# Performance work log

Measured on AMD Instinct MI355X. Metric: run time of the kernel, lower is better.

Reference implementation:

```python
import jax, jax.numpy as jnp
import numpy as np

IN_CH = 128
QK_CH = IN_CH // 8  # 16


def setup_inputs() -> dict:
    key = jax.random.key(0)
    ks = jax.random.split(key, 8)
    B, C, W, H = 8, IN_CH, 64, 64
    x = jax.random.normal(ks[0], (B, C, W, H), dtype=jnp.float32)
    s = 1.0 / np.sqrt(C)
    Wq = jax.random.normal(ks[1], (QK_CH, C), dtype=jnp.float32) * s
    bq = jnp.zeros((QK_CH,), dtype=jnp.float32)
    Wk = jax.random.normal(ks[2], (QK_CH, C), dtype=jnp.float32) * s
    bk = jnp.zeros((QK_CH,), dtype=jnp.float32)
    Wv = jax.random.normal(ks[3], (C, C), dtype=jnp.float32) * s
    bv = jnp.zeros((C,), dtype=jnp.float32)
    gamma = jnp.zeros((1,), dtype=jnp.float32)
    return {"x": x, "Wq": Wq, "bq": bq, "Wk": Wk, "bk": bk, "Wv": Wv, "bv": bv, "gamma": gamma}


def reference(x, Wq, bq, Wk, bk, Wv, bv, gamma):
    B, C, W, H = x.shape
    N = W * H
    xf = x.reshape(B, C, N)  # [B,C,N] tokens along spatial dims
    # 1x1 convs == per-pixel linear projections
    q = jnp.einsum('oc,bcn->bno', Wq, xf) + bq          # [B,N,Cq]
    k = jnp.einsum('oc,bcn->bon', Wk, xf) + bk[:, None]  # [B,Cq,N]
    v = jnp.einsum('oc,bcn->bon', Wv, xf) + bv[:, None]  # [B,C,N]
    scale = jnp.sqrt(jnp.asarray(Wq.shape[0], dtype=x.dtype))
    attn = jax.nn.softmax(jnp.einsum('bno,bom->bnm', q, k) / scale, axis=-1)  # [B,N,N]
    # out[b,c,i] = sum_j v[b,c,j] * attn[b,i,j]  (torch: bmm(value, attention^T))
    out = jnp.einsum('bcj,bij->bci', v, attn).reshape(B, C, W, H)
    return gamma[0] * out + x
```

## Files before the change

kernel.cpp:

```cpp
#include <hip/hip_runtime.h>
#include <cstddef>
#include <cstdint>

#define NTOK 4096
#define NB_  8

typedef float f32x4  __attribute__((ext_vector_type(4)));
typedef float f32x16 __attribute__((ext_vector_type(16)));
typedef short s16x8  __attribute__((ext_vector_type(8)));

static __device__ __forceinline__ unsigned short f2bf(float f) {
    unsigned u = __float_as_uint(f);
    unsigned r = (u + 0x7FFFu + ((u >> 16) & 1u)) >> 16;
    return (unsigned short)r;
}
static __device__ __forceinline__ unsigned packbf2(float a, float b) {
    const unsigned ua = __float_as_uint(a) + 0x8000u;
    const unsigned ub = __float_as_uint(b) + 0x8000u;
    return __builtin_amdgcn_perm(ub, ua, 0x07060302u);
}

__global__ __launch_bounds__(256) void wcvt_kernel(
    const float* __restrict__ Wq, const float* __restrict__ Wk, const float* __restrict__ Wv,
    unsigned short* __restrict__ wvb, unsigned short* __restrict__ wqb,
    unsigned short* __restrict__ wkb)
{
    int i = blockIdx.x * 256 + threadIdx.x;
    if (i < 16384)      wvb[i]         = f2bf(Wv[i]);
    else if (i < 18432) wqb[i - 16384] = f2bf(Wq[i - 16384]);
    else                wkb[i - 18432] = f2bf(Wk[i - 18432]);
}

__global__ __launch_bounds__(256) void proj_kernel(
    const float* __restrict__ x,
    const unsigned short* __restrict__ wvb, const unsigned short* __restrict__ wqb,
    const unsigned short* __restrict__ wkb,
    const float* __restrict__ bq, const float* __restrict__ bk, const float* __restrict__ bv,
    unsigned short* __restrict__ qb, unsigned short* __restrict__ kb,
    unsigned short* __restrict__ vt)
{
    __shared__ float lt[128][68];
    const int t = threadIdx.x;
    const int w = t >> 6, lane = t & 63;
    const int c16 = lane & 15, g16 = lane >> 4;
    const int b  = blockIdx.x & 7;
    const int n0 = (blockIdx.x >> 3) * 64;

    {
        const int n4 = t & 15;
#pragma unroll
        for (int pass = 0; pass < 8; ++pass) {
            const int c = (t >> 4) + 16 * pass;
            const float4 val = ((const float4*)(x + ((size_t)b * 128 + c) * NTOK + n0))[n4];
            *(float4*)&lt[c][n4 * 4] = val;
        }
    }
    __syncthreads();

    const int nl = 16 * w + c16;
    s16x8 xf[4];
#pragma unroll
    for (int kc = 0; kc < 4; ++kc) {
        unsigned rr[8];
#pragma unroll
        for (int i = 0; i < 8; ++i) {
            const unsigned u = __float_as_uint(lt[32 * kc + 8 * g16 + i][nl]);
            rr[i] = u + 0x7FFFu + ((u >> 16) & 1u);
        }
        union { s16x8 v; unsigned u[4]; } cvt;
#pragma unroll
        for (int d = 0; d < 4; ++d)
            cvt.u[d] = __builtin_amdgcn_perm(rr[2 * d + 1], rr[2 * d], 0x07060302u);
        xf[kc] = cvt.v;
    }

    unsigned short* vwp = vt + (size_t)b * (NTOK * 128) +
                          (size_t)(((n0 >> 6) * 8) + 2 * w + (c16 >> 3)) * 1024 + (c16 & 7);
#pragma unroll
    for (int mt = 0; mt < 8; ++mt) {
        f32x4 acc = {0.f, 0.f, 0.f, 0.f};
#pragma unroll
        for (int kc = 0; kc < 4; ++kc) {
            const s16x8 wf = *(const s16x8*)(wvb + (size_t)(16 * mt + c16) * 128 + 32 * kc + 8 * g16);
            acc = __builtin_amdgcn_mfma_f32_16x16x32_bf16(wf, xf[kc], acc, 0, 0, 0);
        }
        const float4 bvv = *(const float4*)(bv + 16 * mt + 4 * g16);
#pragma unroll
        for (int r = 0; r < 4; ++r) {
            const int c = 16 * mt + 4 * g16 + r;
            vwp[c * 8] = f2bf(acc[r] + ((const float*)&bvv)[r]);
        }
    }
    f32x4 aq = {0.f, 0.f, 0.f, 0.f}, ak = {0.f, 0.f, 0.f, 0.f};
#pragma unroll
    for (int kc = 0; kc < 4; ++kc) {
        const s16x8 wqf = *(const s16x8*)(wqb + (size_t)c16 * 128 + 32 * kc + 8 * g16);
        const s16x8 wkf = *(const s16x8*)(wkb + (size_t)c16 * 128 + 32 * kc + 8 * g16);
        aq = __builtin_amdgcn_mfma_f32_16x16x32_bf16(xf[kc], wqf, aq, 0, 0, 0);
        ak = __builtin_amdgcn_mfma_f32_16x16x32_bf16(xf[kc], wkf, ak, 0, 0, 0);
    }
    const float bqv = bq[c16], bkv = bk[c16];
#pragma unroll
    for (int r = 0; r < 4; ++r) {
        const int n = n0 + 16 * w + 4 * g16 + r;
        qb[((size_t)b * NTOK + n) * 16 + c16] = f2bf(0.25f * (aq[r] + bqv));
        kb[((size_t)b * NTOK + n) * 16 + c16] = f2bf(ak[r] + bkv);
    }
}

__global__ __launch_bounds__(256, 2) void flash_kernel(
    const unsigned short* __restrict__ qb, const unsigned short* __restrict__ kb,
    const unsigned short* __restrict__ vt, const float* __restrict__ x,
    const float* __restrict__ gamma, float* __restrict__ out)
{
    __shared__ float smem[4256];

    const int t = threadIdx.x;
    const int w = t >> 6, lane = t & 63;
    const int m31 = lane & 31, h = lane >> 5;
    const int b  = blockIdx.x & 7;
    const int m0 = (blockIdx.x >> 3) * 32;

    const unsigned short* kbb = kb + ((size_t)b * NTOK + w * 1024) * 16;
    const unsigned short* vtb = vt + (size_t)b * (NTOK * 128) + (size_t)w * 16 * 8192 +
                                h * 1024 + m31 * 8;

    const s16x8 qf = *(const s16x8*)(qb + ((size_t)b * NTOK + m0 + m31) * 16 + 8 * h);

    f32x16 O[4];
#pragma unroll
    for (int ct = 0; ct < 4; ++ct)
#pragma unroll
        for (int r = 0; r < 16; ++r) O[ct][r] = 0.f;
    float l_acc = 0.f;

    s16x8 kf0 = *(const s16x8*)(kbb + (size_t)m31 * 16 + 8 * h);
    s16x8 kf1 = *(const s16x8*)(kbb + (size_t)(32 + m31) * 16 + 8 * h);

    const int xaddr = (lane ^ 32) << 2;

    for (int jt = 0; jt < 16; ++jt) {
        const int j0 = jt * 64;

        s16x8 vf[4][4];
#pragma unroll
        for (int s = 0; s < 4; ++s)
#pragma unroll
            for (int ct = 0; ct < 4; ++ct)
                vf[ct][s] = *(const s16x8*)(vtb + jt * 8192 + s * 2048 + ct * 256);

        f32x16 sd[2];
#pragma unroll
        for (int r = 0; r < 16; ++r) { sd[0][r] = 0.f; sd[1][r] = 0.f; }
        sd[0] = __builtin_amdgcn_mfma_f32_32x32x16_bf16(kf0, qf, sd[0], 0, 0, 0);
        sd[1] = __builtin_amdgcn_mfma_f32_32x32x16_bf16(kf1, qf, sd[1], 0, 0, 0);

        if (jt < 15) {
            kf0 = *(const s16x8*)(kbb + (size_t)(j0 + 64 + m31) * 16 + 8 * h);
            kf1 = *(const s16x8*)(kbb + (size_t)(j0 + 96 + m31) * 16 + 8 * h);
        }

#pragma unroll
        for (int t2 = 0; t2 < 2; ++t2)
#pragma unroll
            for (int r = 0; r < 16; ++r) {
                const float e = __expf(sd[t2][r]);
                sd[t2][r] = e;
                l_acc += e;
            }

        uint2 pk[2][4];
#pragma unroll
        for (int t2 = 0; t2 < 2; ++t2)
#pragma unroll
            for (int q = 0; q < 4; ++q) {
                pk[t2][q].x = packbf2(sd[t2][4 * q + 0], sd[t2][4 * q + 1]);
                pk[t2][q].y = packbf2(sd[t2][4 * q + 2], sd[t2][4 * q + 3]);
            }

        uint2 ex[2][2];
#pragma unroll
        for (int t2 = 0; t2 < 2; ++t2)
#pragma unroll
            for (int s1 = 0; s1 < 2; ++s1) {
                const uint2 snd = h ? pk[t2][2 * s1] : pk[t2][2 * s1 + 1];
                ex[t2][s1].x = (unsigned)__builtin_amdgcn_ds_bpermute(xaddr, (int)snd.x);
                ex[t2][s1].y = (unsigned)__builtin_amdgcn_ds_bpermute(xaddr, (int)snd.y);
            }

        s16x8 pf[4];
#pragma unroll
        for (int s = 0; s < 4; ++s) {
            const int t2 = s >> 1, s1 = s & 1;
            const uint2 lo = h ? ex[t2][s1] : pk[t2][2 * s1];
            const uint2 hi = h ? pk[t2][2 * s1 + 1] : ex[t2][s1];
            union { s16x8 v; unsigned u[4]; } asm_;
            asm_.u[0] = lo.x; asm_.u[1] = lo.y; asm_.u[2] = hi.x; asm_.u[3] = hi.y;
            pf[s] = asm_.v;
        }

#pragma unroll
        for (int s = 0; s < 4; ++s)
#pragma unroll
            for (int ct = 0; ct < 4; ++ct)
                O[ct] = __builtin_amdgcn_mfma_f32_32x32x16_bf16(vf[ct][s], pf[s], O[ct], 0, 0, 0);
    }

    l_acc += __shfl_xor(l_acc, 32);

    float* ob = smem;
    float* lb = smem + 4224;
#pragma unroll 1
    for (int src = 1; src < 4; ++src) {
        __syncthreads();
        if (w == src) {
#pragma unroll
            for (int ct = 0; ct < 4; ++ct)
#pragma unroll
                for (int r = 0; r < 16; ++r) {
                    const int c = 32 * ct + (r & 3) + 8 * (r >> 2) + 4 * h;
                    ob[c * 33 + m31] = O[ct][r];
                }
            if (lane < 32) lb[lane] = l_acc;
        }
        __syncthreads();
        if (w == 0) {
#pragma unroll
            for (int ct = 0; ct < 4; ++ct)
#pragma unroll
                for (int r = 0; r < 16; ++r) {
                    const int c = 32 * ct + (r & 3) + 8 * (r >> 2) + 4 * h;
                    O[ct][r] += ob[c * 33 + m31];
                }
            l_acc += lb[m31];
        }
    }

    if (w == 0) {
        const float linv = 1.f / l_acc;
        const float g = gamma[0];
#pragma unroll
        for (int ct = 0; ct < 4; ++ct)
#pragma unroll
            for (int r = 0; r < 16; ++r) {
                const int c = 32 * ct + (r & 3) + 8 * (r >> 2) + 4 * h;
                const size_t idx = ((size_t)b * 128 + c) * NTOK + m0 + m31;
                out[idx] = fmaf(g, O[ct][r] * linv, x[idx]);
            }
    }
}

extern "C" void kernel_launch(void* const* d_in, const int* in_sizes, int n_in,
                              void* d_out, int out_size, void* d_ws, size_t ws_size,
                              hipStream_t stream)
{
    const float* x     = (const float*)d_in[0];
    const float* Wq    = (const float*)d_in[1];
    const float* bq    = (const float*)d_in[2];
    const float* Wk    = (const float*)d_in[3];
    const float* bk    = (const float*)d_in[4];
    const float* Wv    = (const float*)d_in[5];
    const float* bv    = (const float*)d_in[6];
    const float* gamma = (const float*)d_in[7];
    float* out = (float*)d_out;

    unsigned short* qb  = (unsigned short*)d_ws;
    unsigned short* kb  = qb  + (size_t)NB_ * NTOK * 16;
    unsigned short* vt  = kb  + (size_t)NB_ * NTOK * 16;
    unsigned short* wvb = vt  + (size_t)NB_ * 128 * NTOK;
    unsigned short* wqb = wvb + 16384;
    unsigned short* wkb = wqb + 2048;

    wcvt_kernel<<<80, 256, 0, stream>>>(Wq, Wk, Wv, wvb, wqb, wkb);
    proj_kernel<<<512, 256, 0, stream>>>(x, wvb, wqb, wkb, bq, bk, bv, qb, kb, vt);
    flash_kernel<<<1024, 256, 0, stream>>>(qb, kb, vt, x, gamma, out);
}
```

Measured before the change: 208.9 us.

## Split flash attention across channel tiles per wave instead of key ranges

Each of the four waves now owns one 32-channel slice of the output and iterates over all 4096 keys, instead of each wave covering a quarter of the keys for all 128 channels. This removes the shared-memory cross-wave reduction and its barriers, and shrinks the per-wave accumulator from four 32x32 tiles to one. The cost is that the QK^T score MFMAs and the exponentials are recomputed four times, once per wave, and each wave runs a loop four times longer.

```diff
diff --git a/kernel.cpp b/kernel.cpp
--- a/kernel.cpp
+++ b/kernel.cpp
@@ -113,25 +113,21 @@
     const unsigned short* __restrict__ vt, const float* __restrict__ x,
     const float* __restrict__ gamma, float* __restrict__ out)
 {
-    __shared__ float smem[4256];
-
     const int t = threadIdx.x;
     const int w = t >> 6, lane = t & 63;
     const int m31 = lane & 31, h = lane >> 5;
     const int b  = blockIdx.x & 7;
     const int m0 = (blockIdx.x >> 3) * 32;
 
-    const unsigned short* kbb = kb + ((size_t)b * NTOK + w * 1024) * 16;
-    const unsigned short* vtb = vt + (size_t)b * (NTOK * 128) + (size_t)w * 16 * 8192 +
+    const unsigned short* kbb = kb + (size_t)b * NTOK * 16;
+    const unsigned short* vtb = vt + (size_t)b * (NTOK * 128) + w * 256 +
                                 h * 1024 + m31 * 8;
 
     const s16x8 qf = *(const s16x8*)(qb + ((size_t)b * NTOK + m0 + m31) * 16 + 8 * h);
 
-    f32x16 O[4];
-#pragma unroll
-    for (int ct = 0; ct < 4; ++ct)
-#pragma unroll
-        for (int r = 0; r < 16; ++r) O[ct][r] = 0.f;
+    f32x16 O;
+#pragma unroll
+    for (int r = 0; r < 16; ++r) O[r] = 0.f;
     float l_acc = 0.f;
 
     s16x8 kf0 = *(const s16x8*)(kbb + (size_t)m31 * 16 + 8 * h);
@@ -139,15 +135,13 @@
 
     const int xaddr = (lane ^ 32) << 2;
 
-    for (int jt = 0; jt < 16; ++jt) {
+    for (int jt = 0; jt < 64; ++jt) {
         const int j0 = jt * 64;
 
-        s16x8 vf[4][4];
+        s16x8 vf[4];
 #pragma unroll
         for (int s = 0; s < 4; ++s)
-#pragma unroll
-            for (int ct = 0; ct < 4; ++ct)
-                vf[ct][s] = *(const s16x8*)(vtb + jt * 8192 + s * 2048 + ct * 256);
+            vf[s] = *(const s16x8*)(vtb + jt * 8192 + s * 2048);
 
         f32x16 sd[2];
 #pragma unroll
@@ -155,7 +149,7 @@
         sd[0] = __builtin_amdgcn_mfma_f32_32x32x16_bf16(kf0, qf, sd[0], 0, 0, 0);
         sd[1] = __builtin_amdgcn_mfma_f32_32x32x16_bf16(kf1, qf, sd[1], 0, 0, 0);
 
-        if (jt < 15) {
+        if (jt < 63) {
             kf0 = *(const s16x8*)(kbb + (size_t)(j0 + 64 + m31) * 16 + 8 * h);
             kf1 = *(const s16x8*)(kbb + (size_t)(j0 + 96 + m31) * 16 + 8 * h);
         }
@@ -201,52 +195,18 @@
 
 #pragma unroll
         for (int s = 0; s < 4; ++s)
-#pragma unroll
-            for (int ct = 0; ct < 4; ++ct)
-                O[ct] = __builtin_amdgcn_mfma_f32_32x32x16_bf16(vf[ct][s], pf[s], O[ct], 0, 0, 0);
+            O = __builtin_amdgcn_mfma_f32_32x32x16_bf16(vf[s], pf[s], O, 0, 0, 0);
     }
 
     l_acc += __shfl_xor(l_acc, 32);
 
-    float* ob = smem;
-    float* lb = smem + 4224;
-#pragma unroll 1
-    for (int src = 1; src < 4; ++src) {
-        __syncthreads();
-        if (w == src) {
-#pragma unroll
-            for (int ct = 0; ct < 4; ++ct)
-#pragma unroll
-                for (int r = 0; r < 16; ++r) {
-                    const int c = 32 * ct + (r & 3) + 8 * (r >> 2) + 4 * h;
-                    ob[c * 33 + m31] = O[ct][r];
-                }
-            if (lane < 32) lb[lane] = l_acc;
-        }
-        __syncthreads();
-        if (w == 0) {
-#pragma unroll
-            for (int ct = 0; ct < 4; ++ct)
-#pragma unroll
-                for (int r = 0; r < 16; ++r) {
-                    const int c = 32 * ct + (r & 3) + 8 * (r >> 2) + 4 * h;
-                    O[ct][r] += ob[c * 33 + m31];
-                }
-            l_acc += lb[m31];
-        }
-    }
-
-    if (w == 0) {
-        const float linv = 1.f / l_acc;
-        const float g = gamma[0];
-#pragma unroll
-        for (int ct = 0; ct < 4; ++ct)
-#pragma unroll
-            for (int r = 0; r < 16; ++r) {
-                const int c = 32 * ct + (r & 3) + 8 * (r >> 2) + 4 * h;
-                const size_t idx = ((size_t)b * 128 + c) * NTOK + m0 + m31;
-                out[idx] = fmaf(g, O[ct][r] * linv, x[idx]);
-            }
+    const float linv = 1.f / l_acc;
+    const float g = gamma[0];
+#pragma unroll
+    for (int r = 0; r < 16; ++r) {
+        const int c = 32 * w + (r & 3) + 8 * (r >> 2) + 4 * h;
+        const size_t idx = ((size_t)b * 128 + c) * NTOK + m0 + m31;
+        out[idx] = fmaf(g, O[r] * linv, x[idx]);
     }
 }
 
```

Result: slower. 384.9 us (+84.3%).
